# Kernel tuning notes

Measured on AMD Instinct MI355X. Metric: run time of the kernel, lower is better.

Reference implementation:

```python
import jax, jax.numpy as jnp
import numpy as np

T, D, DFF = 8192, 512, 2048
EPS = 1e-5
LS_INIT = 1e-4

def setup_inputs() -> dict:
    key = jax.random.key(0)
    ks = jax.random.split(key, 5)
    s = 0.02
    return {
        "x": jax.random.normal(ks[0], (T, D), jnp.float32),
        "W_in": jax.random.normal(ks[1], (3 * D, D), jnp.float32) * s,
        "W_out": jax.random.normal(ks[2], (D, D), jnp.float32) * s,
        "W1": jax.random.normal(ks[3], (DFF, D), jnp.float32) * s,
        "W2": jax.random.normal(ks[4], (D, DFF), jnp.float32) * s,
        "g1": jnp.ones((D,), jnp.float32),
        "b1": jnp.zeros((D,), jnp.float32),
        "g2": jnp.ones((D,), jnp.float32),
        "b2": jnp.zeros((D,), jnp.float32),
        "ls1": jnp.full((D,), LS_INIT, jnp.float32),
        "ls2": jnp.full((D,), LS_INIT, jnp.float32),
    }

def _layer_norm(x, g, b):
    mu = jnp.mean(x, axis=-1, keepdims=True)
    var = jnp.mean((x - mu) ** 2, axis=-1, keepdims=True)
    return (x - mu) * jax.lax.rsqrt(var + EPS) * g + b

def reference(x, W_in, W_out, W1, W2, g1, b1, g2, b2, ls1, ls2):
    t = x.shape[0]
    # --- self-attention block (faithful: no head split, no 1/sqrt(d) scale, k @ q^T) ---
    h = _layer_norm(x, g1, b1)                       # [T, D]
    proj = h @ W_in.T                                # [T, 3D]
    q, k, v = jnp.split(proj, 3, axis=-1)            # each [T, D]
    scores = k @ q.T                                 # [T, T]
    mask = jnp.tril(jnp.ones((t, t), scores.dtype))
    scores = jnp.where(mask == 0, -jnp.inf, scores)
    attn = jax.nn.softmax(scores, axis=-1)
    o = (attn @ v) @ W_out.T                         # [T, D]
    x = x + ls1 * o
    # --- FFN block ---
    h = _layer_norm(x, g2, b2)
    update = jax.nn.gelu(h @ W1.T) @ W2.T            # [T, D]
    return x + ls2 * update
```

## Files before the change

kernel.cpp:

```cpp
#include <hip/hip_runtime.h>
#include <hip/hip_bf16.h>


using bf16 = __hip_bfloat16;
typedef __attribute__((ext_vector_type(8))) short short8;
typedef __attribute__((ext_vector_type(4))) float f32x4;

#define T_DIM 8192

#define AS1C(p) (const __attribute__((address_space(1))) void*)(p)
#define AS3P(p) (__attribute__((address_space(3))) void*)(p)
#define GLL16(src, dst) __builtin_amdgcn_global_load_lds(AS1C(src), AS3P(dst), 16, 0, 0)

static __device__ __forceinline__ short f2bfbits(float f) {
  bf16 b = __float2bfloat16(f);
  short s; __builtin_memcpy(&s, &b, 2); return s;
}
static __device__ __forceinline__ float bfbits2f(short s) {
  unsigned u = ((unsigned)(unsigned short)s) << 16;
  float f; __builtin_memcpy(&f, &u, 4); return f;
}

__global__ void cvt_kernel(const float* __restrict__ in, bf16* __restrict__ out, int n) {
  int i = blockIdx.x * 256 + threadIdx.x;
  if (i < n) out[i] = __float2bfloat16(in[i]);
}

__global__ __launch_bounds__(256) void ln_kernel(
    const float* __restrict__ x, const float* __restrict__ g,
    const float* __restrict__ bb, bf16* __restrict__ h)
{
  const int row = blockIdx.x * 4 + (threadIdx.x >> 6);
  const int lane = threadIdx.x & 63;
  const float* xr = x + (size_t)row * 512 + lane * 8;
  f32x4 v0 = *(const f32x4*)xr;
  f32x4 v1 = *(const f32x4*)(xr + 4);
  float s = 0.f;
#pragma unroll
  for (int j = 0; j < 4; ++j) s += v0[j] + v1[j];
#pragma unroll
  for (int d = 1; d < 64; d <<= 1) s += __shfl_xor(s, d);
  const float mu = s * (1.f / 512.f);
  float vs = 0.f;
#pragma unroll
  for (int j = 0; j < 4; ++j) { float a = v0[j] - mu, b2 = v1[j] - mu; vs += a * a + b2 * b2; }
#pragma unroll
  for (int d = 1; d < 64; d <<= 1) vs += __shfl_xor(vs, d);
  const float rs = rsqrtf(vs * (1.f / 512.f) + 1e-5f);
  const f32x4 g0 = *(const f32x4*)(g + lane * 8);
  const f32x4 g1v = *(const f32x4*)(g + lane * 8 + 4);
  const f32x4 b0 = *(const f32x4*)(bb + lane * 8);
  const f32x4 b1v = *(const f32x4*)(bb + lane * 8 + 4);
  short8 ov;
#pragma unroll
  for (int j = 0; j < 4; ++j) {
    ov[j]     = f2bfbits((v0[j] - mu) * rs * g0[j] + b0[j]);
    ov[j + 4] = f2bfbits((v1[j] - mu) * rs * g1v[j] + b1v[j]);
  }
  *(short8*)(h + (size_t)row * 512 + lane * 8) = ov;
}

enum { MODE_BF16 = 0, MODE_GELU = 1, MODE_RESID = 2 };

static __device__ __forceinline__ float gelu_f(float x) {
  float x3 = x * x * x;
  float t = tanhf(0.7978845608028654f * (x + 0.044715f * x3));
  return 0.5f * x * (1.0f + t);
}

template <int MODE>
__global__ __launch_bounds__(256, 2) void gemm_bt(
    const bf16* __restrict__ A, const bf16* __restrict__ B,
    int M, int N, int K,
    bf16* __restrict__ Cb, float* __restrict__ Cf,
    const float* __restrict__ resid, const float* __restrict__ scale)
{
  __shared__ bf16 sA[128 * 64];
  __shared__ bf16 sB[128 * 64];
  const int tid = threadIdx.x;
  const int lane = tid & 63, wave = tid >> 6;
  const int bm = blockIdx.x, bn = blockIdx.y;
  const int wm = (wave & 1) * 64, wn = (wave >> 1) * 64;
  const int ln = lane & 15, lg = lane >> 4;
  f32x4 acc[4][4] = {};

  const int nkt = K >> 6;
  for (int kt = 0; kt < nkt; ++kt) {
    __syncthreads();
#pragma unroll
    for (int r = 0; r < 4; ++r) {
      const int s = r * 256 + tid;
      const int ks = s >> 9, rb = (s >> 6) & 7, l = s & 63;
      const bf16* srcA = A + (size_t)(bm * 128 + rb * 16 + (l & 15)) * K + kt * 64 + ks * 32 + (l >> 4) * 8;
      GLL16(srcA, sA + (size_t)(r * 256 + wave * 64) * 8);
      const bf16* srcB = B + (size_t)(bn * 128 + rb * 16 + (l & 15)) * K + kt * 64 + ks * 32 + (l >> 4) * 8;
      GLL16(srcB, sB + (size_t)(r * 256 + wave * 64) * 8);
    }
    __syncthreads();
#pragma unroll
    for (int ks = 0; ks < 2; ++ks) {
      short8 af[4], bfr[4];
#pragma unroll
      for (int mi = 0; mi < 4; ++mi)
        af[mi] = *(const short8*)(sA + (size_t)(ks * 512 + ((wm >> 4) + mi) * 64 + lane) * 8);
#pragma unroll
      for (int ni = 0; ni < 4; ++ni)
        bfr[ni] = *(const short8*)(sB + (size_t)(ks * 512 + ((wn >> 4) + ni) * 64 + lane) * 8);
#pragma unroll
      for (int mi = 0; mi < 4; ++mi)
#pragma unroll
        for (int ni = 0; ni < 4; ++ni)
          acc[mi][ni] = __builtin_amdgcn_mfma_f32_16x16x32_bf16(af[mi], bfr[ni], acc[mi][ni], 0, 0, 0);
    }
  }
#pragma unroll
  for (int mi = 0; mi < 4; ++mi) {
#pragma unroll
    for (int ni = 0; ni < 4; ++ni) {
#pragma unroll
      for (int r = 0; r < 4; ++r) {
        const int row = bm * 128 + wm + mi * 16 + lg * 4 + r;
        const int col = bn * 128 + wn + ni * 16 + ln;
        const size_t idx = (size_t)row * N + col;
        float v = acc[mi][ni][r];
        if constexpr (MODE == MODE_GELU) { Cb[idx] = __float2bfloat16(gelu_f(v)); }
        else if constexpr (MODE == MODE_RESID) { Cf[idx] = resid[idx] + scale[col] * v; }
        else { Cb[idx] = __float2bfloat16(v); }
      }
    }
  }
}

__global__ __launch_bounds__(256) void transpose_v(const bf16* __restrict__ proj, bf16* __restrict__ vT) {
  __shared__ bf16 tile[64][66];
  const int t0 = blockIdx.x * 64, d0 = blockIdx.y * 64;
  const int tid = threadIdx.x;
#pragma unroll
  for (int i = 0; i < 16; ++i) {
    const int lin = i * 256 + tid;
    const int r = lin >> 6, c = lin & 63;
    tile[r][c] = proj[(size_t)(t0 + r) * 1536 + 1024 + d0 + c];
  }
  __syncthreads();
#pragma unroll
  for (int i = 0; i < 16; ++i) {
    const int lin = i * 256 + tid;
    const int dy = lin >> 6, tx = lin & 63;
    vT[(size_t)(d0 + dy) * T_DIM + t0 + tx] = tile[tx][dy];
  }
}

__global__ __launch_bounds__(512, 2) void attn_kernel(
    const bf16* __restrict__ proj, const bf16* __restrict__ vT,
    bf16* __restrict__ Op, float* __restrict__ mlp)
{
  __shared__ bf16 sQ[2][32 * 512];
  __shared__ bf16 sV[2][32 * 512];
  __shared__ bf16 sP[8][16 * 40];

  const int tid = threadIdx.x, lane = tid & 63, wave = tid >> 6;
  const int ln = lane & 15, lg = lane >> 4;
  const int b = 511 - blockIdx.x;
  const int it = b >> 3;
  const int ch = b & 7;
  const int nj = 4 * it + 4;
  const int jlo = ch * nj / 8;
  const int jhi = (ch + 1) * nj / 8;
  const int wrow = it * 128 + wave * 16;

  short8 kf[16];
#pragma unroll
  for (int ks = 0; ks < 16; ++ks)
    kf[ks] = *(const short8*)(proj + (size_t)(wrow + ln) * 1536 + 512 + ks * 32 + lg * 8);

  f32x4 oa[32] = {};
  float m_r[4] = {-__builtin_inff(), -__builtin_inff(), -__builtin_inff(), -__builtin_inff()};
  float l_r[4] = {0.f, 0.f, 0.f, 0.f};

  auto stage = [&](int c, int jt) {
    const int j0 = jt * 32;
#pragma unroll
    for (int r = 0; r < 4; ++r) {
      const int s = r * 512 + tid;
      const int l = s & 63;
      const int ks = s >> 7, jb = (s >> 6) & 1;
      const bf16* srcQ = proj + (size_t)(j0 + jb * 16 + (l & 15)) * 1536 + ks * 32 + (l >> 4) * 8;
      GLL16(srcQ, &sQ[c][(size_t)(r * 512 + wave * 64) * 8]);
      const int nb = s >> 6;
      const bf16* srcV = vT + (size_t)(nb * 16 + (l & 15)) * T_DIM + j0 + (l >> 4) * 8;
      GLL16(srcV, &sV[c][(size_t)(r * 512 + wave * 64) * 8]);
    }
  };

  if (jlo < jhi) {
    int cur = 0;
    stage(0, jlo);
    __syncthreads();

    for (int jt = jlo; jt < jhi; ++jt) {
      const int j0 = jt * 32;
      if (jt + 1 < jhi) stage(cur ^ 1, jt + 1);
      if (j0 <= wrow + 15) {
        f32x4 sfr[2] = {};
#pragma unroll
        for (int ks = 0; ks < 16; ++ks) {
          short8 q0 = *(const short8*)(&sQ[cur][(size_t)(ks * 128 + lane) * 8]);
          short8 q1 = *(const short8*)(&sQ[cur][(size_t)(ks * 128 + 64 + lane) * 8]);
          sfr[0] = __builtin_amdgcn_mfma_f32_16x16x32_bf16(kf[ks], q0, sfr[0], 0, 0, 0);
          sfr[1] = __builtin_amdgcn_mfma_f32_16x16x32_bf16(kf[ks], q1, sfr[1], 0, 0, 0);
        }
        if (j0 + 31 > wrow) {
#pragma unroll
          for (int jb = 0; jb < 2; ++jb)
#pragma unroll
            for (int r = 0; r < 4; ++r) {
              const int i = wrow + lg * 4 + r, j = j0 + jb * 16 + ln;
              if (j > i) sfr[jb][r] = -__builtin_inff();
            }
        }
        float mx[4], sc[4], mm[4];
#pragma unroll
        for (int r = 0; r < 4; ++r) mx[r] = fmaxf(sfr[0][r], sfr[1][r]);
#pragma unroll
        for (int d = 1; d < 16; d <<= 1)
#pragma unroll
          for (int r = 0; r < 4; ++r) mx[r] = fmaxf(mx[r], __shfl_xor(mx[r], d));
#pragma unroll
        for (int r = 0; r < 4; ++r) {
          mm[r] = fmaxf(fmaxf(m_r[r], mx[r]), -1e30f);
          sc[r] = __expf(m_r[r] - mm[r]);
          m_r[r] = mm[r];
          l_r[r] *= sc[r];
        }
        float ts[4] = {0.f, 0.f, 0.f, 0.f};
#pragma unroll
        for (int jb = 0; jb < 2; ++jb)
#pragma unroll
          for (int r = 0; r < 4; ++r) {
            float p = __expf(sfr[jb][r] - mm[r]);
            sfr[jb][r] = p;
            ts[r] += p;
          }
#pragma unroll
        for (int d = 1; d < 16; d <<= 1)
#pragma unroll
          for (int r = 0; r < 4; ++r) ts[r] += __shfl_xor(ts[r], d);
#pragma unroll
        for (int r = 0; r < 4; ++r) l_r[r] += ts[r];
#pragma unroll
        for (int jb = 0; jb < 2; ++jb)
#pragma unroll
          for (int r = 0; r < 4; ++r)
            sP[wave][(lg * 4 + r) * 40 + jb * 16 + ln] = __float2bfloat16(sfr[jb][r]);
#pragma unroll
        for (int nb = 0; nb < 32; ++nb)
#pragma unroll
          for (int r = 0; r < 4; ++r) oa[nb][r] *= sc[r];
        const short8 pa = *(const short8*)(&sP[wave][0] + ln * 40 + lg * 8);
#define LDV(nb) (*(const short8*)(&sV[cur][(size_t)((nb) * 64 + lane) * 8]))
        short8 vf0 = LDV(0), vf1 = LDV(1), vf2 = LDV(2), vf3 = LDV(3);
#pragma unroll
        for (int nb = 0; nb < 28; nb += 4) {
          const short8 w0 = vf0, w1 = vf1, w2 = vf2, w3 = vf3;
          vf0 = LDV(nb + 4); vf1 = LDV(nb + 5); vf2 = LDV(nb + 6); vf3 = LDV(nb + 7);
          oa[nb]     = __builtin_amdgcn_mfma_f32_16x16x32_bf16(pa, w0, oa[nb],     0, 0, 0);
          oa[nb + 1] = __builtin_amdgcn_mfma_f32_16x16x32_bf16(pa, w1, oa[nb + 1], 0, 0, 0);
          oa[nb + 2] = __builtin_amdgcn_mfma_f32_16x16x32_bf16(pa, w2, oa[nb + 2], 0, 0, 0);
          oa[nb + 3] = __builtin_amdgcn_mfma_f32_16x16x32_bf16(pa, w3, oa[nb + 3], 0, 0, 0);
        }
        oa[28] = __builtin_amdgcn_mfma_f32_16x16x32_bf16(pa, vf0, oa[28], 0, 0, 0);
        oa[29] = __builtin_amdgcn_mfma_f32_16x16x32_bf16(pa, vf1, oa[29], 0, 0, 0);
        oa[30] = __builtin_amdgcn_mfma_f32_16x16x32_bf16(pa, vf2, oa[30], 0, 0, 0);
        oa[31] = __builtin_amdgcn_mfma_f32_16x16x32_bf16(pa, vf3, oa[31], 0, 0, 0);
#undef LDV
      }
      __syncthreads();
      cur ^= 1;
    }
  }
#pragma unroll
  for (int nb = 0; nb < 32; ++nb)
#pragma unroll
    for (int r = 0; r < 4; ++r)
      Op[((size_t)ch * T_DIM + wrow + lg * 4 + r) * 512 + nb * 16 + ln] = __float2bfloat16(oa[nb][r]);
  if (ln == 0) {
#pragma unroll
    for (int r = 0; r < 4; ++r) {
      mlp[((size_t)ch * T_DIM + wrow + lg * 4 + r) * 2 + 0] = m_r[r];
      mlp[((size_t)ch * T_DIM + wrow + lg * 4 + r) * 2 + 1] = l_r[r];
    }
  }
}

__global__ __launch_bounds__(256) void combine_kernel(
    const bf16* __restrict__ Op, const float* __restrict__ mlp, bf16* __restrict__ o)
{
  const int row = blockIdx.x * 4 + (threadIdx.x >> 6);
  const int lane = threadIdx.x & 63;
  const int k = 8;
  float m = -__builtin_inff();
  for (int c = 0; c < k; ++c) m = fmaxf(m, mlp[((size_t)c * T_DIM + row) * 2]);
  float l = 0.f;
  for (int c = 0; c < k; ++c) {
    const float mc = mlp[((size_t)c * T_DIM + row) * 2];
    const float lc = mlp[((size_t)c * T_DIM + row) * 2 + 1];
    l += __expf(mc - m) * lc;
  }
  const float inv = 1.0f / l;
  f32x4 a0 = {}, a1 = {};
  for (int c = 0; c < k; ++c) {
    const float w = __expf(mlp[((size_t)c * T_DIM + row) * 2] - m);
    const short8 u = *(const short8*)(Op + ((size_t)c * T_DIM + row) * 512 + lane * 8);
#pragma unroll
    for (int j = 0; j < 4; ++j) {
      a0[j] += w * bfbits2f(u[j]);
      a1[j] += w * bfbits2f(u[j + 4]);
    }
  }
  short8 ov;
#pragma unroll
  for (int j = 0; j < 4; ++j) {
    ov[j]     = f2bfbits(a0[j] * inv);
    ov[j + 4] = f2bfbits(a1[j] * inv);
  }
  *(short8*)(o + (size_t)row * 512 + lane * 8) = ov;
}

extern "C" void kernel_launch(void* const* d_in, const int* in_sizes, int n_in,
                              void* d_out, int out_size, void* d_ws, size_t ws_size,
                              hipStream_t stream) {
  (void)in_sizes; (void)n_in; (void)out_size; (void)ws_size;
  const float* x    = (const float*)d_in[0];
  const float* Win  = (const float*)d_in[1];
  const float* Wout = (const float*)d_in[2];
  const float* W1   = (const float*)d_in[3];
  const float* W2   = (const float*)d_in[4];
  const float* g1   = (const float*)d_in[5];
  const float* b1   = (const float*)d_in[6];
  const float* g2   = (const float*)d_in[7];
  const float* b2   = (const float*)d_in[8];
  const float* ls1  = (const float*)d_in[9];
  const float* ls2  = (const float*)d_in[10];
  float* out = (float*)d_out;

  char* w = (char*)d_ws;
  size_t off = 0;
  auto alloc = [&](size_t bytes) -> char* {
    char* p = w + off; off += (bytes + 255) & ~(size_t)255; return p;
  };
  bf16* wWin  = (bf16*)alloc((size_t)1536 * 512 * 2);
  bf16* wWout = (bf16*)alloc((size_t)512 * 512 * 2);
  bf16* wW1   = (bf16*)alloc((size_t)2048 * 512 * 2);
  bf16* wW2   = (bf16*)alloc((size_t)512 * 2048 * 2);
  bf16* h     = (bf16*)alloc((size_t)T_DIM * 512 * 2);
  bf16* proj  = (bf16*)alloc((size_t)T_DIM * 1536 * 2);
  bf16* vTb   = (bf16*)alloc((size_t)512 * T_DIM * 2);
  bf16* o     = (bf16*)alloc((size_t)T_DIM * 512 * 2);
  float* x1   = (float*)alloc((size_t)T_DIM * 512 * 4);
  bf16* Op    = (bf16*)alloc((size_t)8 * T_DIM * 512 * 2);
  float* mlp  = (float*)alloc((size_t)8 * T_DIM * 2 * 4);
  bf16* f1 = proj;

  cvt_kernel<<<1536 * 512 / 256, 256, 0, stream>>>(Win, wWin, 1536 * 512);
  cvt_kernel<<<512 * 512 / 256, 256, 0, stream>>>(Wout, wWout, 512 * 512);
  cvt_kernel<<<2048 * 512 / 256, 256, 0, stream>>>(W1, wW1, 2048 * 512);
  cvt_kernel<<<512 * 2048 / 256, 256, 0, stream>>>(W2, wW2, 512 * 2048);

  ln_kernel<<<T_DIM / 4, 256, 0, stream>>>(x, g1, b1, h);
  gemm_bt<MODE_BF16><<<dim3(64, 12), 256, 0, stream>>>(h, wWin, 8192, 1536, 512, proj, nullptr, nullptr, nullptr);
  transpose_v<<<dim3(T_DIM / 64, 8), 256, 0, stream>>>(proj, vTb);
  attn_kernel<<<512, 512, 0, stream>>>(proj, vTb, Op, mlp);
  combine_kernel<<<T_DIM / 4, 256, 0, stream>>>(Op, mlp, o);
  gemm_bt<MODE_RESID><<<dim3(64, 4), 256, 0, stream>>>(o, wWout, 8192, 512, 512, nullptr, x1, x, ls1);
  ln_kernel<<<T_DIM / 4, 256, 0, stream>>>(x1, g2, b2, h);
  gemm_bt<MODE_GELU><<<dim3(64, 16), 256, 0, stream>>>(h, wW1, 8192, 2048, 512, f1, nullptr, nullptr, nullptr);
  gemm_bt<MODE_RESID><<<dim3(64, 4), 256, 0, stream>>>(f1, wW2, 8192, 512, 2048, nullptr, out, x1, ls2);
}
```

Before: 376.8 us.

## Split attention Q/V staging with finer waitcnt barriers and merge weight conversions

The attention loop now issues the Q-tile and V-tile async LDS loads separately. It uses explicit vmcnt waits and raw barriers, so the next Q tile loads during the current QK step and the next V tile loads after the softmax. This replaces the single end-of-iteration __syncthreads with two finer sync points, and adds s_setprio around the MFMA loops. The four weight-conversion launches are merged into one kernel to cut launch overhead. The hand-counted vmcnt values are fragile: if the outstanding-load counts don't match the compiler's emitted loads, the kernel races.

```diff
diff --git a/kernel.cpp b/kernel.cpp
--- a/kernel.cpp
+++ b/kernel.cpp
@@ -21,9 +21,20 @@
   float f; __builtin_memcpy(&f, &u, 4); return f;
 }
 
-__global__ void cvt_kernel(const float* __restrict__ in, bf16* __restrict__ out, int n) {
+__global__ void cvt4_kernel(
+    const float* __restrict__ a, bf16* __restrict__ oa, int na,
+    const float* __restrict__ b, bf16* __restrict__ ob, int nb,
+    const float* __restrict__ c, bf16* __restrict__ oc, int nc,
+    const float* __restrict__ d, bf16* __restrict__ od, int nd)
+{
   int i = blockIdx.x * 256 + threadIdx.x;
-  if (i < n) out[i] = __float2bfloat16(in[i]);
+  if (i < na) { oa[i] = __float2bfloat16(a[i]); return; }
+  i -= na;
+  if (i < nb) { ob[i] = __float2bfloat16(b[i]); return; }
+  i -= nb;
+  if (i < nc) { oc[i] = __float2bfloat16(c[i]); return; }
+  i -= nc;
+  if (i < nd) od[i] = __float2bfloat16(d[i]);
 }
 
 __global__ __launch_bounds__(256) void ln_kernel(
@@ -177,7 +188,7 @@
   float m_r[4] = {-__builtin_inff(), -__builtin_inff(), -__builtin_inff(), -__builtin_inff()};
   float l_r[4] = {0.f, 0.f, 0.f, 0.f};
 
-  auto stage = [&](int c, int jt) {
+  auto stageQ = [&](int c, int jt) {
     const int j0 = jt * 32;
 #pragma unroll
     for (int r = 0; r < 4; ++r) {
@@ -186,6 +197,14 @@
       const int ks = s >> 7, jb = (s >> 6) & 1;
       const bf16* srcQ = proj + (size_t)(j0 + jb * 16 + (l & 15)) * 1536 + ks * 32 + (l >> 4) * 8;
       GLL16(srcQ, &sQ[c][(size_t)(r * 512 + wave * 64) * 8]);
+    }
+  };
+  auto stageV = [&](int c, int jt) {
+    const int j0 = jt * 32;
+#pragma unroll
+    for (int r = 0; r < 4; ++r) {
+      const int s = r * 512 + tid;
+      const int l = s & 63;
       const int nb = s >> 6;
       const bf16* srcV = vT + (size_t)(nb * 16 + (l & 15)) * T_DIM + j0 + (l >> 4) * 8;
       GLL16(srcV, &sV[c][(size_t)(r * 512 + wave * 64) * 8]);
@@ -194,14 +213,19 @@
 
   if (jlo < jhi) {
     int cur = 0;
-    stage(0, jlo);
-    __syncthreads();
-
+    stageQ(0, jlo);
+    stageV(0, jlo);
     for (int jt = jlo; jt < jhi; ++jt) {
       const int j0 = jt * 32;
-      if (jt + 1 < jhi) stage(cur ^ 1, jt + 1);
+      const bool more = (jt + 1 < jhi);
+      if (more) stageQ(cur ^ 1, jt + 1);
+      if (more) { asm volatile("s_waitcnt vmcnt(8)" ::: "memory"); }
+      else      { asm volatile("s_waitcnt vmcnt(4)" ::: "memory"); }
+      __builtin_amdgcn_s_barrier();
+      __builtin_amdgcn_sched_barrier(0);
       if (j0 <= wrow + 15) {
         f32x4 sfr[2] = {};
+        __builtin_amdgcn_s_setprio(1);
 #pragma unroll
         for (int ks = 0; ks < 16; ++ks) {
           short8 q0 = *(const short8*)(&sQ[cur][(size_t)(ks * 128 + lane) * 8]);
@@ -209,6 +233,7 @@
           sfr[0] = __builtin_amdgcn_mfma_f32_16x16x32_bf16(kf[ks], q0, sfr[0], 0, 0, 0);
           sfr[1] = __builtin_amdgcn_mfma_f32_16x16x32_bf16(kf[ks], q1, sfr[1], 0, 0, 0);
         }
+        __builtin_amdgcn_s_setprio(0);
         if (j0 + 31 > wrow) {
 #pragma unroll
           for (int jb = 0; jb < 2; ++jb)
@@ -256,7 +281,15 @@
         for (int nb = 0; nb < 32; ++nb)
 #pragma unroll
           for (int r = 0; r < 4; ++r) oa[nb][r] *= sc[r];
+      }
+      if (more) stageV(cur ^ 1, jt + 1);
+      if (more) { asm volatile("s_waitcnt vmcnt(8)" ::: "memory"); }
+      else      { asm volatile("s_waitcnt vmcnt(0)" ::: "memory"); }
+      __builtin_amdgcn_s_barrier();
+      __builtin_amdgcn_sched_barrier(0);
+      if (j0 <= wrow + 15) {
         const short8 pa = *(const short8*)(&sP[wave][0] + ln * 40 + lg * 8);
+        __builtin_amdgcn_s_setprio(1);
 #define LDV(nb) (*(const short8*)(&sV[cur][(size_t)((nb) * 64 + lane) * 8]))
         short8 vf0 = LDV(0), vf1 = LDV(1), vf2 = LDV(2), vf3 = LDV(3);
 #pragma unroll
@@ -273,8 +306,8 @@
         oa[30] = __builtin_amdgcn_mfma_f32_16x16x32_bf16(pa, vf2, oa[30], 0, 0, 0);
         oa[31] = __builtin_amdgcn_mfma_f32_16x16x32_bf16(pa, vf3, oa[31], 0, 0, 0);
 #undef LDV
+        __builtin_amdgcn_s_setprio(0);
       }
-      __syncthreads();
       cur ^= 1;
     }
   }
@@ -361,10 +394,9 @@
   float* mlp  = (float*)alloc((size_t)8 * T_DIM * 2 * 4);
   bf16* f1 = proj;
 
-  cvt_kernel<<<1536 * 512 / 256, 256, 0, stream>>>(Win, wWin, 1536 * 512);
-  cvt_kernel<<<512 * 512 / 256, 256, 0, stream>>>(Wout, wWout, 512 * 512);
-  cvt_kernel<<<2048 * 512 / 256, 256, 0, stream>>>(W1, wW1, 2048 * 512);
-  cvt_kernel<<<512 * 2048 / 256, 256, 0, stream>>>(W2, wW2, 512 * 2048);
+  cvt4_kernel<<<(1536 * 512 + 512 * 512 + 2048 * 512 + 512 * 2048 + 255) / 256, 256, 0, stream>>>(
+      Win, wWin, 1536 * 512, Wout, wWout, 512 * 512,
+      W1, wW1, 2048 * 512, W2, wW2, 512 * 2048);
 
   ln_kernel<<<T_DIM / 4, 256, 0, stream>>>(x, g1, b1, h);
   gemm_bt<MODE_BF16><<<dim3(64, 12), 256, 0, stream>>>(h, wWin, 8192, 1536, 512, proj, nullptr, nullptr, nullptr);
```

Result: faster. 329.1 us (-12.7%).
